# Performance work log

Measured on AMD Instinct MI355X. Metric: run time of the kernel, lower is better.

Reference implementation:

```python
import jax, jax.numpy as jnp
import numpy as np

B, C, Q, E, H = 8, 1024, 128, 512, 1024


def setup_inputs() -> dict:
    key = jax.random.key(0)
    ks = jax.random.split(key, 8)
    return {
        "context": jax.random.normal(ks[0], (B, C, E), jnp.float32),
        "question": jax.random.normal(ks[1], (B, Q, E), jnp.float32),
        "context_mask": jnp.ones((B, C), jnp.float32),
        "w_question": jax.random.normal(ks[2], (E,), jnp.float32),
        "w_context": jax.random.normal(ks[3], (E,), jnp.float32),
        "w_multiple": jax.random.normal(ks[4], (E,), jnp.float32),
        "W1": jax.random.normal(ks[5], (4 * E, H), jnp.float32) * 0.02,
        "b1": jnp.zeros((H,), jnp.float32),
        "W2": jax.random.normal(ks[6], (H, 4 * E), jnp.float32) * 0.02,
        "b2": jnp.zeros((4 * E,), jnp.float32),
    }


def reference(context, question, context_mask, w_question, w_context, w_multiple, W1, b1, W2, b2):
    # Dropout is identity at eval time.
    # Trilinear similarity: s[b,c,q] = q.w_q + ctx.w_c + sum_e q_e*ctx_e*w_m_e
    q_w = question @ w_question                                  # (B,Q)
    c_w = context @ w_context                                    # (B,C)
    mult = jnp.einsum("bqe,bce->bcq", question * w_multiple, context)  # avoids (B,C,Q,E)
    sim = q_w[:, None, :] + c_w[:, :, None] + mult               # (B,C,Q)

    # Context2Query: softmax over question dim (dim=2)
    c2q = jnp.einsum("bcq,bqe->bce", jax.nn.softmax(sim, axis=2), question)
    # Query2Context: max over question dim, softmax over context dim (dim=1)
    q2c = jnp.einsum("bc,bce->be", jax.nn.softmax(jnp.max(sim, axis=2), axis=1), context)  # (B,E)

    attended = jnp.concatenate(
        [context, c2q, context * c2q, context * q2c[:, None, :]], axis=2
    )  # (B,C,4E)

    # MaskedLinear: linear then zero out masked context positions
    m = context_mask[:, :, None]
    h = (attended @ W1 + b1) * m
    out = jax.nn.relu((h @ W2 + b2) * m)
    return out
```

## Files before the change

kernel.cpp:

```cpp
#include <hip/hip_runtime.h>

typedef __bf16 bf16;
typedef __bf16 bf16x4 __attribute__((ext_vector_type(4)));
typedef __bf16 bf16x8 __attribute__((ext_vector_type(8)));
typedef float f32x4 __attribute__((ext_vector_type(4)));
typedef float f32x16 __attribute__((ext_vector_type(16)));

#define AS1 __attribute__((address_space(1)))
#define AS3 __attribute__((address_space(3)))

__device__ __forceinline__ void async_copy16(const void* g, void* l) {
  __builtin_amdgcn_global_load_lds((const AS1 void*)g, (AS3 void*)l, 16, 0, 0);
}

#define BB 8
#define CC 1024
#define QQ 128
#define EE 512
#define HH 1024
#define FOURE 2048

__global__ __launch_bounds__(256) void prep_kernel(
    const float* __restrict__ W1, const float* __restrict__ W2,
    const float* __restrict__ qst, const float* __restrict__ wmul,
    const float* __restrict__ wqv, bf16* __restrict__ W1T,
    bf16* __restrict__ W2T, bf16* __restrict__ qT,
    bf16* __restrict__ qmh, bf16* __restrict__ qml, float* __restrict__ qw) {
  __shared__ float tile[32][33];
  __shared__ float r4[4];
  int bx = blockIdx.x;
  int t = threadIdx.x;
  if (bx >= 4608) {
    int i = bx - 4608;
    int half = t >> 7, tr = t & 127;
    int rowg = i * 2 + half;
    const float* qrow = qst + (size_t)rowg * EE;
    float4 qv = *(const float4*)&qrow[tr * 4];
    float4 wm4 = *(const float4*)&wmul[tr * 4];
    float4 wq4 = *(const float4*)&wqv[tr * 4];
    float m[4] = {qv.x * wm4.x, qv.y * wm4.y, qv.z * wm4.z, qv.w * wm4.w};
    bf16x4 h, l;
#pragma unroll
    for (int k = 0; k < 4; ++k) {
      bf16 hh = (bf16)m[k];
      h[k] = hh; l[k] = (bf16)(m[k] - (float)hh);
    }
    *(bf16x4*)&qmh[(size_t)rowg * EE + tr * 4] = h;
    *(bf16x4*)&qml[(size_t)rowg * EE + tr * 4] = l;
    float s = qv.x * wq4.x + qv.y * wq4.y + qv.z * wq4.z + qv.w * wq4.w;
#pragma unroll
    for (int off = 32; off; off >>= 1) s += __shfl_xor(s, off);
    if ((t & 63) == 0) r4[t >> 6] = s;
    __syncthreads();
    if (tr == 0) qw[rowg] = r4[half * 2] + r4[half * 2 + 1];
    return;
  }
  const float* src;
  bf16* dst;
  int R, C, idx;
  if (bx < 2048) {
    src = W1; dst = W1T; R = 2048; C = 1024; idx = bx;
  } else if (bx < 4096) {
    src = W2; dst = W2T; R = 1024; C = 2048; idx = bx - 2048;
  } else {
    int i = bx - 4096;
    int b = i >> 6; idx = i & 63;
    src = qst + (size_t)b * QQ * EE; dst = qT + (size_t)b * EE * QQ;
    R = 128; C = 512;
  }
  int ctiles = C >> 5;
  int by = idx / ctiles, cx = idx % ctiles;
  int tx = t & 31, ty = t >> 5;
#pragma unroll
  for (int rr = 0; rr < 4; ++rr)
    tile[ty + rr * 8][tx] = src[(size_t)(by * 32 + ty + rr * 8) * C + cx * 32 + tx];
  __syncthreads();
#pragma unroll
  for (int rr = 0; rr < 4; ++rr)
    dst[(size_t)(cx * 32 + ty + rr * 8) * R + by * 32 + tx] = (bf16)tile[tx][ty + rr * 8];
}

__global__ __launch_bounds__(256) void sim_kernel(
    const float* __restrict__ ctx, const bf16* __restrict__ qmh,
    const bf16* __restrict__ qml, const float* __restrict__ wc,
    const float* __restrict__ qw, bf16* __restrict__ P,
    float* __restrict__ smax) {
  int b = blockIdx.y;
  int m0 = blockIdx.x * 64;
  __shared__ bf16 Ah[64 * 32], Al[64 * 32], Bh[128 * 32], Bl[128 * 32];
  __shared__ float wc_s[EE];
  __shared__ float qw_s[QQ];
  __shared__ float cw_s[64];
  __shared__ float sim_s[64][132];
  int t = threadIdx.x;
  for (int i = t; i < EE; i += 256) wc_s[i] = wc[i];
  if (t < QQ) qw_s[t] = qw[b * QQ + t];
  __syncthreads();
  int wv = t >> 6, ln = t & 63, wm = wv >> 1, wn = wv & 1;
  f32x4 acc[2][4] = {};
  const float* Ag = ctx + ((size_t)b * CC + m0) * EE;
  const bf16* Bhg = qmh + (size_t)b * QQ * EE;
  const bf16* Blg = qml + (size_t)b * QQ * EE;
  int arow = t >> 2, acq = t & 3;
  float cwp = 0.f;
  for (int k0 = 0; k0 < EE; k0 += 32) {
    {
      const float4* s4 = (const float4*)(Ag + (size_t)arow * EE + k0 + acq * 8);
      float4 v0 = s4[0], v1 = s4[1];
      float vals[8] = {v0.x, v0.y, v0.z, v0.w, v1.x, v1.y, v1.z, v1.w};
      bf16x8 h, l;
#pragma unroll
      for (int i = 0; i < 8; ++i) {
        cwp += vals[i] * wc_s[k0 + acq * 8 + i];
        bf16 hh = (bf16)vals[i];
        h[i] = hh; l[i] = (bf16)(vals[i] - (float)hh);
      }
      int sl = (acq ^ ((arow >> 1) & 3)) * 8;
      *(bf16x8*)&Ah[arow * 32 + sl] = h;
      *(bf16x8*)&Al[arow * 32 + sl] = l;
    }
#pragma unroll
    for (int r = 0; r < 2; ++r) {
      int fb = (r * 4 + wv) * 1024 + ln * 16;
      int row = fb >> 6;
      int cq = ((fb >> 4) & 3) ^ ((row >> 1) & 3);
      async_copy16(Bhg + (size_t)row * EE + k0 + cq * 8, (char*)Bh + fb);
      async_copy16(Blg + (size_t)row * EE + k0 + cq * 8, (char*)Bl + fb);
    }
    __syncthreads();
    int rl = ln & 15, kq = ln >> 4;
    bf16x8 ah[2], al[2], bh[4], bl[4];
#pragma unroll
    for (int i = 0; i < 2; ++i) {
      int r = wm * 32 + i * 16 + rl;
      int sl = (kq ^ ((r >> 1) & 3)) * 8;
      ah[i] = *(const bf16x8*)&Ah[r * 32 + sl];
      al[i] = *(const bf16x8*)&Al[r * 32 + sl];
    }
#pragma unroll
    for (int j = 0; j < 4; ++j) {
      int r = wn * 64 + j * 16 + rl;
      int sl = (kq ^ ((r >> 1) & 3)) * 8;
      bh[j] = *(const bf16x8*)&Bh[r * 32 + sl];
      bl[j] = *(const bf16x8*)&Bl[r * 32 + sl];
    }
#pragma unroll
    for (int i = 0; i < 2; ++i)
#pragma unroll
      for (int j = 0; j < 4; ++j) {
        acc[i][j] = __builtin_amdgcn_mfma_f32_16x16x32_bf16(ah[i], bh[j], acc[i][j], 0, 0, 0);
        acc[i][j] = __builtin_amdgcn_mfma_f32_16x16x32_bf16(ah[i], bl[j], acc[i][j], 0, 0, 0);
        acc[i][j] = __builtin_amdgcn_mfma_f32_16x16x32_bf16(al[i], bh[j], acc[i][j], 0, 0, 0);
      }
    __syncthreads();
  }
  float s = cwp;
  s += __shfl_xor(s, 1); s += __shfl_xor(s, 2);
  if ((t & 3) == 0) cw_s[arow] = s;
#pragma unroll
  for (int j = 0; j < 4; ++j) {
    int col = wn * 64 + j * 16 + (ln & 15);
    float qv = qw_s[col];
#pragma unroll
    for (int i = 0; i < 2; ++i) {
      int rbase = wm * 32 + i * 16 + ((ln >> 4) << 2);
#pragma unroll
      for (int r = 0; r < 4; ++r)
        sim_s[rbase + r][col] = acc[i][j][r] + qv;
    }
  }
  __syncthreads();
  int row = t >> 2, cb = t & 3;
  float v[32];
  float mx = -3.4e38f;
#pragma unroll
  for (int k = 0; k < 32; ++k) {
    v[k] = sim_s[row][cb + 4 * k];
    mx = fmaxf(mx, v[k]);
  }
  mx = fmaxf(mx, __shfl_xor(mx, 1));
  mx = fmaxf(mx, __shfl_xor(mx, 2));
  float sm = 0.f;
#pragma unroll
  for (int k = 0; k < 32; ++k) { v[k] = __expf(v[k] - mx); sm += v[k]; }
  sm += __shfl_xor(sm, 1);
  sm += __shfl_xor(sm, 2);
  float inv = 1.0f / sm;
  bf16* Pr = P + (size_t)(b * CC + m0 + row) * QQ;
#pragma unroll
  for (int k = 0; k < 32; ++k) Pr[cb + 4 * k] = (bf16)(v[k] * inv);
  if (cb == 0) smax[b * CC + m0 + row] = mx + cw_s[row];
}

__global__ __launch_bounds__(256) void q2c_kernel(
    const float* __restrict__ ctx, const float* __restrict__ smax,
    float* __restrict__ q2c) {
  int b = blockIdx.x >> 5, ch = blockIdx.x & 31;
  int t = threadIdx.x;
  __shared__ float red[256];
  __shared__ float w_s[32];
  float v[4];
  float mx = -3.4e38f;
#pragma unroll
  for (int i = 0; i < 4; ++i) {
    v[i] = smax[b * CC + i * 256 + t];
    mx = fmaxf(mx, v[i]);
  }
  red[t] = mx;
  __syncthreads();
  for (int s = 128; s > 0; s >>= 1) {
    if (t < s) red[t] = fmaxf(red[t], red[t + s]);
    __syncthreads();
  }
  mx = red[0];
  __syncthreads();
  float sm = 0.f;
#pragma unroll
  for (int i = 0; i < 4; ++i) sm += __expf(v[i] - mx);
  red[t] = sm;
  __syncthreads();
  for (int s = 128; s > 0; s >>= 1) {
    if (t < s) red[t] += red[t + s];
    __syncthreads();
  }
  float inv = 1.0f / red[0];
  if (t < 32) w_s[t] = __expf(smax[b * CC + ch * 32 + t] - mx) * inv;
  __syncthreads();
  int e = t * 2;
  const float* cb = ctx + ((size_t)b * CC + ch * 32) * EE;
  float a0 = 0.f, a1 = 0.f;
#pragma unroll 8
  for (int r = 0; r < 32; ++r) {
    float2 vv = *(const float2*)&cb[(size_t)r * EE + e];
    float w = w_s[r];
    a0 += w * vv.x;
    a1 += w * vv.y;
  }
  atomicAdd(&q2c[b * EE + e], a0);
  atomicAdd(&q2c[b * EE + e + 1], a1);
}

template <int MT, int OUT_BF16, int RELU, int HAS_BIAS, int HAS_MASK>
__global__ __launch_bounds__(256) void gemm_bt_kernel(
    const bf16* __restrict__ A, const bf16* __restrict__ Bt,
    const float* __restrict__ bias, const float* __restrict__ mask,
    void* __restrict__ Cout, int M, int N, int K, long sA, long sB, long sC) {
  int b = blockIdx.y;
  A += (size_t)b * sA;
  Bt += (size_t)b * sB;
  int ntiles = N >> 7;
  int mt = blockIdx.x / ntiles, ntb = blockIdx.x % ntiles;
  int m0 = mt * MT, n0 = ntb << 7;
  __shared__ bf16 As[MT * 64];
  __shared__ bf16 Bs[128 * 64];
  int t = threadIdx.x, wv = t >> 6, ln = t & 63;
  int wm = wv >> 1, wn = wv & 1;
  constexpr int MI = MT / 64;
  f32x16 acc[MI][2] = {};
  for (int k0 = 0; k0 < K; k0 += 64) {
#pragma unroll
    for (int r = 0; r < MT / 32; ++r) {
      int fb = (r * 4 + wv) * 1024 + ln * 16;
      int row = fb >> 7;
      int q = ((fb >> 4) & 7) ^ (row & 7);
      async_copy16(A + (size_t)(m0 + row) * K + k0 + q * 8,
                   (char*)As + fb);
    }
#pragma unroll
    for (int r = 0; r < 4; ++r) {
      int fb = (r * 4 + wv) * 1024 + ln * 16;
      int row = fb >> 7;
      int q = ((fb >> 4) & 7) ^ (row & 7);
      async_copy16(Bt + (size_t)(n0 + row) * K + k0 + q * 8,
                   (char*)Bs + fb);
    }
    __syncthreads();
    int rl = ln & 31, kh = ln >> 5;
#pragma unroll
    for (int s = 0; s < 4; ++s) {
      int c = s * 2 + kh;
      bf16x8 af[MI], bfr[2];
#pragma unroll
      for (int i = 0; i < MI; ++i) {
        int row = wm * (MT / 2) + i * 32 + rl;
        af[i] = *(const bf16x8*)&As[row * 64 + ((c ^ (row & 7)) * 8)];
      }
#pragma unroll
      for (int j = 0; j < 2; ++j) {
        int row = wn * 64 + j * 32 + rl;
        bfr[j] = *(const bf16x8*)&Bs[row * 64 + ((c ^ (row & 7)) * 8)];
      }
#pragma unroll
      for (int i = 0; i < MI; ++i)
#pragma unroll
        for (int j = 0; j < 2; ++j)
          acc[i][j] = __builtin_amdgcn_mfma_f32_32x32x16_bf16(af[i], bfr[j], acc[i][j], 0, 0, 0);
    }
    __syncthreads();
  }
  size_t outbase = (size_t)b * sC;
  int lh = ln >> 5;
#pragma unroll
  for (int j = 0; j < 2; ++j) {
    int col = n0 + wn * 64 + j * 32 + (ln & 31);
    float bv = HAS_BIAS ? bias[col] : 0.f;
#pragma unroll
    for (int i = 0; i < MI; ++i) {
      int rbase = m0 + wm * (MT / 2) + i * 32 + 4 * lh;
#pragma unroll
      for (int r = 0; r < 16; ++r) {
        int row = rbase + (r & 3) + 8 * (r >> 2);
        float v = acc[i][j][r] + bv;
        if (HAS_MASK) v *= mask[row];
        if (RELU) v = fmaxf(v, 0.f);
        if (OUT_BF16)
          ((bf16*)Cout)[outbase + (size_t)row * N + col] = (bf16)v;
        else
          ((float*)Cout)[outbase + (size_t)row * N + col] = v;
      }
    }
  }
}

__global__ __launch_bounds__(256) void attbuild_kernel(
    const float* __restrict__ ctx, const bf16* __restrict__ c2q,
    const float* __restrict__ q2c, bf16* __restrict__ att) {
  int idx = blockIdx.x * 256 + threadIdx.x;
  int row = idx >> 7;
  int e = (idx & 127) * 4;
  int b = row >> 10;
  float4 cv = *(const float4*)&ctx[(size_t)row * EE + e];
  bf16x4 qv = *(const bf16x4*)&c2q[(size_t)row * EE + e];
  float4 gv = *(const float4*)&q2c[b * EE + e];
  bf16* dst = att + (size_t)row * FOURE;
  bf16x4 o0, o2, o3;
  o0[0] = (bf16)cv.x; o0[1] = (bf16)cv.y; o0[2] = (bf16)cv.z; o0[3] = (bf16)cv.w;
  o2[0] = (bf16)(cv.x * (float)qv[0]); o2[1] = (bf16)(cv.y * (float)qv[1]);
  o2[2] = (bf16)(cv.z * (float)qv[2]); o2[3] = (bf16)(cv.w * (float)qv[3]);
  o3[0] = (bf16)(cv.x * gv.x); o3[1] = (bf16)(cv.y * gv.y);
  o3[2] = (bf16)(cv.z * gv.z); o3[3] = (bf16)(cv.w * gv.w);
  *(bf16x4*)&dst[e] = o0;
  *(bf16x4*)&dst[512 + e] = qv;
  *(bf16x4*)&dst[1024 + e] = o2;
  *(bf16x4*)&dst[1536 + e] = o3;
}

extern "C" void kernel_launch(void* const* d_in, const int* in_sizes, int n_in,
                              void* d_out, int out_size, void* d_ws, size_t ws_size,
                              hipStream_t stream) {
  const float* ctx = (const float*)d_in[0];
  const float* qst = (const float*)d_in[1];
  const float* mask = (const float*)d_in[2];
  const float* wqv = (const float*)d_in[3];
  const float* wcv = (const float*)d_in[4];
  const float* wmul = (const float*)d_in[5];
  const float* W1 = (const float*)d_in[6];
  const float* b1 = (const float*)d_in[7];
  const float* W2 = (const float*)d_in[8];
  const float* b2 = (const float*)d_in[9];
  float* out = (float*)d_out;
  char* ws = (char*)d_ws;

  bf16* att = (bf16*)(ws);
  bf16* hbuf = (bf16*)(ws + 33554432);
  bf16* W1T = (bf16*)(ws + 50331648);
  bf16* W2T = (bf16*)(ws + 54525952);
  bf16* qT = (bf16*)(ws + 58720256);
  bf16* P = (bf16*)(ws + 59768832);
  bf16* c2q = (bf16*)(ws + 61865984);
  bf16* qmh = (bf16*)(ws + 70254592);
  bf16* qml = (bf16*)(ws + 71303168);
  float* smax = (float*)(ws + 72351744);
  float* q2c = (float*)(ws + 72384512);
  float* qw = (float*)(ws + 72400896);

  prep_kernel<<<5120, 256, 0, stream>>>(W1, W2, qst, wmul, wqv,
                                        W1T, W2T, qT, qmh, qml, qw);
  sim_kernel<<<dim3(16, BB), 256, 0, stream>>>(ctx, qmh, qml, wcv, qw, P, smax);
  hipMemsetAsync(q2c, 0, BB * EE * sizeof(float), stream);
  q2c_kernel<<<256, 256, 0, stream>>>(ctx, smax, q2c);
  gemm_bt_kernel<128, 1, 0, 0, 0><<<dim3(32, BB), 256, 0, stream>>>(
      P, qT, nullptr, nullptr, c2q, 1024, 512, 128,
      (long)CC * QQ, (long)EE * QQ, (long)CC * EE);
  attbuild_kernel<<<4096, 256, 0, stream>>>(ctx, c2q, q2c, att);
  gemm_bt_kernel<64, 1, 0, 1, 1><<<dim3(1024, 1), 256, 0, stream>>>(
      att, W1T, b1, mask, hbuf, 8192, 1024, 2048, 0, 0, 0);
  gemm_bt_kernel<128, 0, 1, 1, 1><<<dim3(1024, 1), 256, 0, stream>>>(
      hbuf, W2T, b2, mask, out, 8192, 2048, 1024, 0, 0, 0);
}
```

Measured before the change: 242.1 us.

## Fuse similarity, softmax, c2q GEMM and attention build; retile big GEMMs

The similarity kernel now also computes the context-to-query product in-block from the softmax tile held in shared memory, and writes the first three quarters of the attended matrix directly. This removes the P and c2q round trips through global memory and two launches, and a small kernel fills the q2c quarter. Separately, the generic GEMM switches from 32x32x16 to 16x16x32 MFMA tiles and uses a grouped block-index swizzle meant to improve L2 reuse. The fused kernel uses 32-row tiles, so only half the threads load A, and the c2q B-fragments are read straight from global memory.

```diff
diff --git a/kernel.cpp b/kernel.cpp
--- a/kernel.cpp
+++ b/kernel.cpp
@@ -4,7 +4,6 @@
 typedef __bf16 bf16x4 __attribute__((ext_vector_type(4)));
 typedef __bf16 bf16x8 __attribute__((ext_vector_type(8)));
 typedef float f32x4 __attribute__((ext_vector_type(4)));
-typedef float f32x16 __attribute__((ext_vector_type(16)));
 
 #define AS1 __attribute__((address_space(1)))
 #define AS3 __attribute__((address_space(3)))
@@ -80,31 +79,38 @@
     dst[(size_t)(cx * 32 + ty + rr * 8) * R + by * 32 + tx] = (bf16)tile[tx][ty + rr * 8];
 }
 
-__global__ __launch_bounds__(256) void sim_kernel(
+__global__ __launch_bounds__(256) void fused_att_kernel(
     const float* __restrict__ ctx, const bf16* __restrict__ qmh,
-    const bf16* __restrict__ qml, const float* __restrict__ wc,
-    const float* __restrict__ qw, bf16* __restrict__ P,
-    float* __restrict__ smax) {
+    const bf16* __restrict__ qml, const bf16* __restrict__ qT,
+    const float* __restrict__ wc, const float* __restrict__ qw,
+    float* __restrict__ smax, bf16* __restrict__ att) {
   int b = blockIdx.y;
-  int m0 = blockIdx.x * 64;
-  __shared__ bf16 Ah[64 * 32], Al[64 * 32], Bh[128 * 32], Bl[128 * 32];
+  int m0 = blockIdx.x * 32;
+  __shared__ __align__(16) char U[37376];
+  bf16* Ah = (bf16*)(U);
+  bf16* Al = (bf16*)(U + 2048);
+  bf16* Bh = (bf16*)(U + 4096);
+  bf16* Bl = (bf16*)(U + 12288);
+  float(*sim_s)[132] = (float(*)[132])(U + 20480);
+  bf16* c2q_lds = (bf16*)(U);
   __shared__ float wc_s[EE];
   __shared__ float qw_s[QQ];
-  __shared__ float cw_s[64];
-  __shared__ float sim_s[64][132];
+  __shared__ float cw_s[32];
+  __shared__ bf16 P_lds[32][136];
   int t = threadIdx.x;
   for (int i = t; i < EE; i += 256) wc_s[i] = wc[i];
   if (t < QQ) qw_s[t] = qw[b * QQ + t];
   __syncthreads();
   int wv = t >> 6, ln = t & 63, wm = wv >> 1, wn = wv & 1;
-  f32x4 acc[2][4] = {};
+  int rl = ln & 15, kq = ln >> 4;
+  f32x4 acc[4] = {};
   const float* Ag = ctx + ((size_t)b * CC + m0) * EE;
   const bf16* Bhg = qmh + (size_t)b * QQ * EE;
   const bf16* Blg = qml + (size_t)b * QQ * EE;
   int arow = t >> 2, acq = t & 3;
   float cwp = 0.f;
   for (int k0 = 0; k0 < EE; k0 += 32) {
-    {
+    if (t < 128) {
       const float4* s4 = (const float4*)(Ag + (size_t)arow * EE + k0 + acq * 8);
       float4 v0 = s4[0], v1 = s4[1];
       float vals[8] = {v0.x, v0.y, v0.z, v0.w, v1.x, v1.y, v1.z, v1.w};
@@ -128,14 +134,12 @@
       async_copy16(Blg + (size_t)row * EE + k0 + cq * 8, (char*)Bl + fb);
     }
     __syncthreads();
-    int rl = ln & 15, kq = ln >> 4;
-    bf16x8 ah[2], al[2], bh[4], bl[4];
-#pragma unroll
-    for (int i = 0; i < 2; ++i) {
-      int r = wm * 32 + i * 16 + rl;
+    bf16x8 ah, al, bh[4], bl[4];
+    {
+      int r = wm * 16 + rl;
       int sl = (kq ^ ((r >> 1) & 3)) * 8;
-      ah[i] = *(const bf16x8*)&Ah[r * 32 + sl];
-      al[i] = *(const bf16x8*)&Al[r * 32 + sl];
+      ah = *(const bf16x8*)&Ah[r * 32 + sl];
+      al = *(const bf16x8*)&Al[r * 32 + sl];
     }
 #pragma unroll
     for (int j = 0; j < 4; ++j) {
@@ -145,51 +149,106 @@
       bl[j] = *(const bf16x8*)&Bl[r * 32 + sl];
     }
 #pragma unroll
-    for (int i = 0; i < 2; ++i)
-#pragma unroll
-      for (int j = 0; j < 4; ++j) {
-        acc[i][j] = __builtin_amdgcn_mfma_f32_16x16x32_bf16(ah[i], bh[j], acc[i][j], 0, 0, 0);
-        acc[i][j] = __builtin_amdgcn_mfma_f32_16x16x32_bf16(ah[i], bl[j], acc[i][j], 0, 0, 0);
-        acc[i][j] = __builtin_amdgcn_mfma_f32_16x16x32_bf16(al[i], bh[j], acc[i][j], 0, 0, 0);
+    for (int j = 0; j < 4; ++j) {
+      acc[j] = __builtin_amdgcn_mfma_f32_16x16x32_bf16(ah, bh[j], acc[j], 0, 0, 0);
+      acc[j] = __builtin_amdgcn_mfma_f32_16x16x32_bf16(ah, bl[j], acc[j], 0, 0, 0);
+      acc[j] = __builtin_amdgcn_mfma_f32_16x16x32_bf16(al, bh[j], acc[j], 0, 0, 0);
+    }
+    __syncthreads();
+  }
+  if (t < 128) {
+    float s = cwp;
+    s += __shfl_xor(s, 1); s += __shfl_xor(s, 2);
+    if ((t & 3) == 0) cw_s[arow] = s;
+  }
+#pragma unroll
+  for (int j = 0; j < 4; ++j) {
+    int col = wn * 64 + j * 16 + rl;
+    float qv = qw_s[col];
+    int rbase = wm * 16 + kq * 4;
+#pragma unroll
+    for (int r = 0; r < 4; ++r) sim_s[rbase + r][col] = acc[j][r] + qv;
+  }
+  __syncthreads();
+  {
+    int row = t >> 3, cb = t & 7;
+    float v[16];
+    float mx = -3.4e38f;
+#pragma unroll
+    for (int k = 0; k < 16; ++k) {
+      v[k] = sim_s[row][cb + 8 * k];
+      mx = fmaxf(mx, v[k]);
+    }
+    mx = fmaxf(mx, __shfl_xor(mx, 1));
+    mx = fmaxf(mx, __shfl_xor(mx, 2));
+    mx = fmaxf(mx, __shfl_xor(mx, 4));
+    float sm = 0.f;
+#pragma unroll
+    for (int k = 0; k < 16; ++k) { v[k] = __expf(v[k] - mx); sm += v[k]; }
+    sm += __shfl_xor(sm, 1);
+    sm += __shfl_xor(sm, 2);
+    sm += __shfl_xor(sm, 4);
+    float inv = 1.0f / sm;
+#pragma unroll
+    for (int k = 0; k < 16; ++k) P_lds[row][cb + 8 * k] = (bf16)(v[k] * inv);
+    if (cb == 0) smax[b * CC + m0 + row] = mx + cw_s[row];
+  }
+  __syncthreads();
+  f32x4 acc2[2][8] = {};
+  const bf16* qTb = qT + (size_t)b * EE * QQ;
+#pragma unroll
+  for (int kk = 0; kk < 4; ++kk) {
+    bf16x8 af2[2];
+#pragma unroll
+    for (int i = 0; i < 2; ++i) {
+      bf16x4 lo = *(const bf16x4*)&P_lds[i * 16 + rl][kk * 32 + kq * 8];
+      bf16x4 hi = *(const bf16x4*)&P_lds[i * 16 + rl][kk * 32 + kq * 8 + 4];
+      af2[i][0] = lo[0]; af2[i][1] = lo[1]; af2[i][2] = lo[2]; af2[i][3] = lo[3];
+      af2[i][4] = hi[0]; af2[i][5] = hi[1]; af2[i][6] = hi[2]; af2[i][7] = hi[3];
+    }
+#pragma unroll
+    for (int j = 0; j < 8; ++j) {
+      int n = wv * 128 + j * 16 + rl;
+      bf16x8 bfr = *(const bf16x8*)&qTb[(size_t)n * QQ + kk * 32 + kq * 8];
+#pragma unroll
+      for (int i = 0; i < 2; ++i)
+        acc2[i][j] = __builtin_amdgcn_mfma_f32_16x16x32_bf16(af2[i], bfr, acc2[i][j], 0, 0, 0);
+    }
+  }
+#pragma unroll
+  for (int j = 0; j < 8; ++j) {
+    int col = wv * 128 + j * 16 + rl;
+#pragma unroll
+    for (int i = 0; i < 2; ++i) {
+      int rbase = i * 16 + kq * 4;
+#pragma unroll
+      for (int r = 0; r < 4; ++r)
+        c2q_lds[(size_t)(rbase + r) * 520 + col] = (bf16)acc2[i][j][r];
+    }
+  }
+  __syncthreads();
+  {
+    int row = t >> 3, c8 = (t & 7) * 64;
+    const float* crow = ctx + ((size_t)(b * CC + m0 + row)) * EE;
+    bf16* arow_p = att + ((size_t)(b * CC + m0 + row)) * FOURE;
+#pragma unroll
+    for (int cc = 0; cc < 8; ++cc) {
+      int col = c8 + cc * 8;
+      bf16x8 q8 = *(const bf16x8*)&c2q_lds[(size_t)row * 520 + col];
+      float4 v0 = *(const float4*)&crow[col];
+      float4 v1 = *(const float4*)&crow[col + 4];
+      float cv[8] = {v0.x, v0.y, v0.z, v0.w, v1.x, v1.y, v1.z, v1.w};
+      bf16x8 o0, o2;
+#pragma unroll
+      for (int k = 0; k < 8; ++k) {
+        o0[k] = (bf16)cv[k];
+        o2[k] = (bf16)(cv[k] * (float)q8[k]);
       }
-    __syncthreads();
-  }
-  float s = cwp;
-  s += __shfl_xor(s, 1); s += __shfl_xor(s, 2);
-  if ((t & 3) == 0) cw_s[arow] = s;
-#pragma unroll
-  for (int j = 0; j < 4; ++j) {
-    int col = wn * 64 + j * 16 + (ln & 15);
-    float qv = qw_s[col];
-#pragma unroll
-    for (int i = 0; i < 2; ++i) {
-      int rbase = wm * 32 + i * 16 + ((ln >> 4) << 2);
-#pragma unroll
-      for (int r = 0; r < 4; ++r)
-        sim_s[rbase + r][col] = acc[i][j][r] + qv;
-    }
-  }
-  __syncthreads();
-  int row = t >> 2, cb = t & 3;
-  float v[32];
-  float mx = -3.4e38f;
-#pragma unroll
-  for (int k = 0; k < 32; ++k) {
-    v[k] = sim_s[row][cb + 4 * k];
-    mx = fmaxf(mx, v[k]);
-  }
-  mx = fmaxf(mx, __shfl_xor(mx, 1));
-  mx = fmaxf(mx, __shfl_xor(mx, 2));
-  float sm = 0.f;
-#pragma unroll
-  for (int k = 0; k < 32; ++k) { v[k] = __expf(v[k] - mx); sm += v[k]; }
-  sm += __shfl_xor(sm, 1);
-  sm += __shfl_xor(sm, 2);
-  float inv = 1.0f / sm;
-  bf16* Pr = P + (size_t)(b * CC + m0 + row) * QQ;
-#pragma unroll
-  for (int k = 0; k < 32; ++k) Pr[cb + 4 * k] = (bf16)(v[k] * inv);
-  if (cb == 0) smax[b * CC + m0 + row] = mx + cw_s[row];
+      *(bf16x8*)&arow_p[col] = o0;
+      *(bf16x8*)&arow_p[EE + col] = q8;
+      *(bf16x8*)&arow_p[2 * EE + col] = o2;
+    }
+  }
 }
 
 __global__ __launch_bounds__(256) void q2c_kernel(
@@ -240,6 +299,25 @@
   atomicAdd(&q2c[b * EE + e + 1], a1);
 }
 
+__global__ __launch_bounds__(256) void att3_kernel(
+    const float* __restrict__ ctx, const float* __restrict__ q2c,
+    bf16* __restrict__ att) {
+  int idx = blockIdx.x * 256 + threadIdx.x;
+  int row = idx >> 6;
+  int e = (idx & 63) * 8;
+  int b = row >> 10;
+  float4 v0 = *(const float4*)&ctx[(size_t)row * EE + e];
+  float4 v1 = *(const float4*)&ctx[(size_t)row * EE + e + 4];
+  float4 g0 = *(const float4*)&q2c[b * EE + e];
+  float4 g1 = *(const float4*)&q2c[b * EE + e + 4];
+  bf16x8 o;
+  o[0] = (bf16)(v0.x * g0.x); o[1] = (bf16)(v0.y * g0.y);
+  o[2] = (bf16)(v0.z * g0.z); o[3] = (bf16)(v0.w * g0.w);
+  o[4] = (bf16)(v1.x * g1.x); o[5] = (bf16)(v1.y * g1.y);
+  o[6] = (bf16)(v1.z * g1.z); o[7] = (bf16)(v1.w * g1.w);
+  *(bf16x8*)&att[(size_t)row * FOURE + 3 * EE + e] = o;
+}
+
 template <int MT, int OUT_BF16, int RELU, int HAS_BIAS, int HAS_MASK>
 __global__ __launch_bounds__(256) void gemm_bt_kernel(
     const bf16* __restrict__ A, const bf16* __restrict__ Bt,
@@ -249,14 +327,16 @@
   A += (size_t)b * sA;
   Bt += (size_t)b * sB;
   int ntiles = N >> 7;
-  int mt = blockIdx.x / ntiles, ntb = blockIdx.x % ntiles;
+  int tiles_per_g = 8 * ntiles;
+  int g = blockIdx.x / tiles_per_g, sub = blockIdx.x % tiles_per_g;
+  int mt = g * 8 + (sub & 7), ntb = sub >> 3;
   int m0 = mt * MT, n0 = ntb << 7;
   __shared__ bf16 As[MT * 64];
   __shared__ bf16 Bs[128 * 64];
   int t = threadIdx.x, wv = t >> 6, ln = t & 63;
   int wm = wv >> 1, wn = wv & 1;
-  constexpr int MI = MT / 64;
-  f32x16 acc[MI][2] = {};
+  constexpr int MI = MT / 32;
+  f32x4 acc[MI][4] = {};
   for (int k0 = 0; k0 < K; k0 += 64) {
 #pragma unroll
     for (int r = 0; r < MT / 32; ++r) {
@@ -275,41 +355,40 @@
                    (char*)Bs + fb);
     }
     __syncthreads();
-    int rl = ln & 31, kh = ln >> 5;
-#pragma unroll
-    for (int s = 0; s < 4; ++s) {
-      int c = s * 2 + kh;
-      bf16x8 af[MI], bfr[2];
+    int rl = ln & 15, kq = ln >> 4;
+#pragma unroll
+    for (int ks = 0; ks < 2; ++ks) {
+      int c = ks * 4 + kq;
+      bf16x8 af[MI], bfr[4];
 #pragma unroll
       for (int i = 0; i < MI; ++i) {
-        int row = wm * (MT / 2) + i * 32 + rl;
+        int row = wm * (MT / 2) + i * 16 + rl;
         af[i] = *(const bf16x8*)&As[row * 64 + ((c ^ (row & 7)) * 8)];
       }
 #pragma unroll
-      for (int j = 0; j < 2; ++j) {
-        int row = wn * 64 + j * 32 + rl;
+      for (int j = 0; j < 4; ++j) {
+        int row = wn * 64 + j * 16 + rl;
         bfr[j] = *(const bf16x8*)&Bs[row * 64 + ((c ^ (row & 7)) * 8)];
       }
 #pragma unroll
       for (int i = 0; i < MI; ++i)
 #pragma unroll
-        for (int j = 0; j < 2; ++j)
-          acc[i][j] = __builtin_amdgcn_mfma_f32_32x32x16_bf16(af[i], bfr[j], acc[i][j], 0, 0, 0);
+        for (int j = 0; j < 4; ++j)
+          acc[i][j] = __builtin_amdgcn_mfma_f32_16x16x32_bf16(af[i], bfr[j], acc[i][j], 0, 0, 0);
     }
     __syncthreads();
   }
   size_t outbase = (size_t)b * sC;
-  int lh = ln >> 5;
-#pragma unroll
-  for (int j = 0; j < 2; ++j) {
-    int col = n0 + wn * 64 + j * 32 + (ln & 31);
+#pragma unroll
+  for (int j = 0; j < 4; ++j) {
+    int col = n0 + wn * 64 + j * 16 + (ln & 15);
     float bv = HAS_BIAS ? bias[col] : 0.f;
 #pragma unroll
     for (int i = 0; i < MI; ++i) {
-      int rbase = m0 + wm * (MT / 2) + i * 32 + 4 * lh;
-#pragma unroll
-      for (int r = 0; r < 16; ++r) {
-        int row = rbase + (r & 3) + 8 * (r >> 2);
+      int rbase = m0 + wm * (MT / 2) + i * 16 + ((ln >> 4) << 2);
+#pragma unroll
+      for (int r = 0; r < 4; ++r) {
+        int row = rbase + r;
         float v = acc[i][j][r] + bv;
         if (HAS_MASK) v *= mask[row];
         if (RELU) v = fmaxf(v, 0.f);
@@ -320,29 +399,6 @@
       }
     }
   }
-}
-
-__global__ __launch_bounds__(256) void attbuild_kernel(
-    const float* __restrict__ ctx, const bf16* __restrict__ c2q,
-    const float* __restrict__ q2c, bf16* __restrict__ att) {
-  int idx = blockIdx.x * 256 + threadIdx.x;
-  int row = idx >> 7;
-  int e = (idx & 127) * 4;
-  int b = row >> 10;
-  float4 cv = *(const float4*)&ctx[(size_t)row * EE + e];
-  bf16x4 qv = *(const bf16x4*)&c2q[(size_t)row * EE + e];
-  float4 gv = *(const float4*)&q2c[b * EE + e];
-  bf16* dst = att + (size_t)row * FOURE;
-  bf16x4 o0, o2, o3;
-  o0[0] = (bf16)cv.x; o0[1] = (bf16)cv.y; o0[2] = (bf16)cv.z; o0[3] = (bf16)cv.w;
-  o2[0] = (bf16)(cv.x * (float)qv[0]); o2[1] = (bf16)(cv.y * (float)qv[1]);
-  o2[2] = (bf16)(cv.z * (float)qv[2]); o2[3] = (bf16)(cv.w * (float)qv[3]);
-  o3[0] = (bf16)(cv.x * gv.x); o3[1] = (bf16)(cv.y * gv.y);
-  o3[2] = (bf16)(cv.z * gv.z); o3[3] = (bf16)(cv.w * gv.w);
-  *(bf16x4*)&dst[e] = o0;
-  *(bf16x4*)&dst[512 + e] = qv;
-  *(bf16x4*)&dst[1024 + e] = o2;
-  *(bf16x4*)&dst[1536 + e] = o3;
 }
 
 extern "C" void kernel_launch(void* const* d_in, const int* in_sizes, int n_in,
@@ -366,23 +422,19 @@
   bf16* W1T = (bf16*)(ws + 50331648);
   bf16* W2T = (bf16*)(ws + 54525952);
   bf16* qT = (bf16*)(ws + 58720256);
-  bf16* P = (bf16*)(ws + 59768832);
-  bf16* c2q = (bf16*)(ws + 61865984);
-  bf16* qmh = (bf16*)(ws + 70254592);
-  bf16* qml = (bf16*)(ws + 71303168);
-  float* smax = (float*)(ws + 72351744);
-  float* q2c = (float*)(ws + 72384512);
-  float* qw = (float*)(ws + 72400896);
+  bf16* qmh = (bf16*)(ws + 59768832);
+  bf16* qml = (bf16*)(ws + 60817408);
+  float* smax = (float*)(ws + 61865984);
+  float* q2c = (float*)(ws + 61898752);
+  float* qw = (float*)(ws + 61915136);
 
   prep_kernel<<<5120, 256, 0, stream>>>(W1, W2, qst, wmul, wqv,
                                         W1T, W2T, qT, qmh, qml, qw);
-  sim_kernel<<<dim3(16, BB), 256, 0, stream>>>(ctx, qmh, qml, wcv, qw, P, smax);
+  fused_att_kernel<<<dim3(32, BB), 256, 0, stream>>>(ctx, qmh, qml, qT, wcv,
+                                                     qw, smax, att);
   hipMemsetAsync(q2c, 0, BB * EE * sizeof(float), stream);
   q2c_kernel<<<256, 256, 0, stream>>>(ctx, smax, q2c);
-  gemm_bt_kernel<128, 1, 0, 0, 0><<<dim3(32, BB), 256, 0, stream>>>(
-      P, qT, nullptr, nullptr, c2q, 1024, 512, 128,
-      (long)CC * QQ, (long)EE * QQ, (long)CC * EE);
-  attbuild_kernel<<<4096, 256, 0, stream>>>(ctx, c2q, q2c, att);
+  att3_kernel<<<2048, 256, 0, stream>>>(ctx, q2c, att);
   gemm_bt_kernel<64, 1, 0, 1, 1><<<dim3(1024, 1), 256, 0, stream>>>(
       att, W1T, b1, mask, hbuf, 8192, 1024, 2048, 0, 0, 0);
   gemm_bt_kernel<128, 0, 1, 1, 1><<<dim3(1024, 1), 256, 0, stream>>>(
```

Measured after the change: 242.6 us. Within noise of the previous version (+0.2%).
